# Optimization experiments

Measured on AMD Instinct MI355X. Metric: run time of the kernel, lower is better.

## Reference

```python
import jax, jax.numpy as jnp
import numpy as np

B, Hs, Ws, ENC = 128, 14, 14, 2048
ATT, EMB, DEC, V, L = 512, 512, 512, 30000, 22


def setup_inputs() -> dict:
    key = jax.random.key(0)
    ks = jax.random.split(key, 16)
    u = lambda k, shape, a: jax.random.uniform(k, shape, jnp.float32, -a, a)
    cap_len_rest = jax.random.randint(ks[2], (B - 1, 1), 2, L + 1)
    caption_lengths = jnp.concatenate([jnp.array([[L]], dtype=cap_len_rest.dtype), cap_len_rest], axis=0)
    return {
        "encoder_out": jax.random.normal(ks[0], (B, Hs, Ws, ENC), jnp.float32),
        "encoded_captions": jax.random.randint(ks[1], (B, L), 0, V),
        "caption_lengths": caption_lengths,
        # learned parameters
        "emb_table": u(ks[3], (V, EMB), 0.1),
        "We": u(ks[4], (ENC, ATT), 0.02), "be": jnp.zeros((ATT,), jnp.float32),
        "Wd": u(ks[5], (DEC, ATT), 0.02), "bd": jnp.zeros((ATT,), jnp.float32),
        "wf": u(ks[6], (ATT,), 0.02), "bf": jnp.zeros((), jnp.float32),
        "W_ih": u(ks[7], (4 * DEC, EMB + ENC), 0.02), "b_ih": jnp.zeros((4 * DEC,), jnp.float32),
        "W_hh": u(ks[8], (4 * DEC, DEC), 0.02), "b_hh": jnp.zeros((4 * DEC,), jnp.float32),
        "W_fc": u(ks[9], (DEC, V), 0.1), "b_fc": jnp.zeros((V,), jnp.float32),
    }


def reference(encoder_out, encoded_captions, caption_lengths,
              emb_table, We, be, Wd, bd, wf, bf,
              W_ih, b_ih, W_hh, b_hh, W_fc, b_fc):
    Bsz = encoder_out.shape[0]
    enc = encoder_out.reshape(Bsz, -1, encoder_out.shape[-1])  # [B, P, ENC]
    lens = caption_lengths[:, 0]
    sort_ind = jnp.argsort(-lens)  # descending, stable
    lens = lens[sort_ind]
    enc = enc[sort_ind]
    caps = encoded_captions[sort_ind]
    emb = emb_table[caps]  # [B, L, EMB]
    dec_lens = lens - 1
    T = caps.shape[1] - 1  # static max(decode_lengths) (max length present in batch)
    D = W_hh.shape[1]

    attn1 = enc @ We + be  # [B, P, ATT], loop-invariant
    h0 = jnp.zeros((Bsz, D), enc.dtype)
    c0 = jnp.zeros((Bsz, D), enc.dtype)

    def step(carry, xs):
        h, c = carry
        emb_t, active = xs  # [B, EMB], [B] bool
        attn2 = h @ Wd + bd  # [B, ATT]
        e = jnp.einsum('bpa,a->bp', jax.nn.relu(attn1 + attn2[:, None, :]), wf) + bf
        alpha = jax.nn.softmax(e, axis=1)  # [B, P]
        ctx = jnp.einsum('bp,bpe->be', alpha, enc)  # [B, ENC]
        x = jnp.concatenate([emb_t, ctx], axis=1)
        gates = x @ W_ih.T + b_ih + h @ W_hh.T + b_hh
        i, f, g, o = jnp.split(gates, 4, axis=1)  # PyTorch LSTM gate order
        c_new = jax.nn.sigmoid(f) * c + jax.nn.sigmoid(i) * jnp.tanh(g)
        h_new = jax.nn.sigmoid(o) * jnp.tanh(c_new)
        m = active[:, None]
        h = jnp.where(m, h_new, h)
        c = jnp.where(m, c_new, c)
        out_t = jnp.where(m, h_new @ W_fc + b_fc, 0.0)  # [B, V]
        alpha_t = jnp.where(m, alpha, 0.0)
        return (h, c), (out_t, alpha_t)

    ts = jnp.arange(T)
    active = ts[:, None] < dec_lens[None, :]  # [T, B]
    emb_steps = jnp.transpose(emb[:, :T], (1, 0, 2))  # [T, B, EMB]
    (_, _), (outs, alphas) = jax.lax.scan(step, (h0, c0), (emb_steps, active))
    outputs = jnp.transpose(outs, (1, 0, 2))  # [B, T, V]
    alphas = jnp.transpose(alphas, (1, 0, 2))  # [B, T, P]
    return outputs, caps, dec_lens, alphas, sort_ind
```

## Files before the change

kernel.cpp:

```cpp
#include <hip/hip_runtime.h>
#include <cstdint>
#include <cstddef>

#define B_    128
#define P_    196
#define ENC_  2048
#define ATT_  512
#define DEC_  512
#define EMB_  512
#define V_    30000
#define VPAD_ 30080
#define L_    22
#define T_    21
#define KGATE (EMB_ + ENC_ + DEC_)
#define NGATE (4*DEC_)
#define KS    8
#define LDSK  40

typedef unsigned short u16;
typedef unsigned int   u32;
typedef float f32x4 __attribute__((ext_vector_type(4)));
typedef short s16x8 __attribute__((ext_vector_type(8)));

__device__ __forceinline__ u16 f2bf(float f){
  u32 u = __float_as_uint(f);
  u = (u + 0x7fffu + ((u >> 16) & 1u)) >> 16;
  return (u16)u;
}
__device__ __forceinline__ float bf2f(u16 h){
  return __uint_as_float(((u32)h) << 16);
}

__device__ __forceinline__ void gload_lds16(const u16* g, u16* l){
  __builtin_amdgcn_global_load_lds(
      (const __attribute__((address_space(1))) void*)g,
      (__attribute__((address_space(3))) void*)l, 16, 0, 0);
}

template<int MODE>
__global__ __launch_bounds__(256)
void gemm_bt(const u16* __restrict__ A,
             const u16* __restrict__ Bt,
             int N, int K,
             const float* __restrict__ bias,
             u16* __restrict__ outb,
             float* __restrict__ outp,
             const int* __restrict__ declens)
{
  __shared__ __align__(16) char smem[32768];
  u16 (*As)[128*32] = reinterpret_cast<u16(*)[128*32]>(smem);
  u16 (*Bs)[128*32] = reinterpret_cast<u16(*)[128*32]>(smem + 16384);
  float* Cs = reinterpret_cast<float*>(smem);

  const int tid = threadIdx.x;

  const int nwg = gridDim.x * gridDim.y;
  int lin = blockIdx.y * gridDim.x + blockIdx.x;
  {
    int q = nwg >> 3, r = nwg & 7;
    int xcd = lin & 7, idx = lin >> 3;
    lin = (xcd < r ? xcd * (q + 1) : r * (q + 1) + (xcd - r) * q) + idx;
  }
  int bxn, bym;
  if (MODE == 2){ bym = lin % gridDim.x; bxn = lin / gridDim.x; }
  else          { bxn = lin % gridDim.x; bym = lin / gridDim.x; }
  const int nt = bxn * 128;
  const size_t mt = (size_t)bym * 128;

  const int wv = tid >> 6;
  const int ln = tid & 63;
  const int lm = ln & 15;
  const int qd = ln >> 4;
  const int wr = wv >> 1;
  const int wc = wv & 1;

  f32x4 acc[4][4];
  #pragma unroll
  for (int i=0;i<4;i++)
    #pragma unroll
    for (int j=0;j<4;j++) acc[i][j] = f32x4{0.f,0.f,0.f,0.f};

  const int c0 = tid, c1 = 256 + tid;
  const int ar0 = c0 >> 2, ac0 = (((c0 & 3) ^ ((ar0 >> 1) & 3)) * 8);
  const int ar1 = c1 >> 2, ac1 = (((c1 & 3) ^ ((ar1 >> 1) & 3)) * 8);
  const u16* Ab0 = A  + (mt + ar0) * (size_t)K + ac0;
  const u16* Ab1 = A  + (mt + ar1) * (size_t)K + ac1;
  const u16* Bb0 = Bt + ((size_t)nt + ar0) * (size_t)K + ac0;
  const u16* Bb1 = Bt + ((size_t)nt + ar1) * (size_t)K + ac1;
  const int lo0 = c0 * 8, lo1 = c1 * 8;

  int aoff[4], boff[4];
  #pragma unroll
  for (int i=0;i<4;i++){
    int ra = wr*64 + i*16 + lm;
    aoff[i] = ra*32 + ((qd ^ ((ra >> 1) & 3)) * 8);
    int rb = wc*64 + i*16 + lm;
    boff[i] = rb*32 + ((qd ^ ((rb >> 1) & 3)) * 8);
  }

#define STAGE_(buf, kc) do {                       \
    gload_lds16(Ab0 + (kc), &As[buf][lo0]);        \
    gload_lds16(Ab1 + (kc), &As[buf][lo1]);        \
    gload_lds16(Bb0 + (kc), &Bs[buf][lo0]);        \
    gload_lds16(Bb1 + (kc), &Bs[buf][lo1]);        \
  } while(0)

  STAGE_(0, 0);
  __syncthreads();
  int cur = 0;
  for (int kc = 0; kc < K; kc += 32){
    if (kc + 32 < K) STAGE_(cur ^ 1, kc + 32);
    s16x8 af[4], bfr[4];
    #pragma unroll
    for (int i=0;i<4;i++) af[i]  = *reinterpret_cast<const s16x8*>(&As[cur][aoff[i]]);
    #pragma unroll
    for (int i=0;i<4;i++) bfr[i] = *reinterpret_cast<const s16x8*>(&Bs[cur][boff[i]]);
    #pragma unroll
    for (int i=0;i<4;i++)
      #pragma unroll
      for (int j=0;j<4;j++)
        acc[i][j] = __builtin_amdgcn_mfma_f32_16x16x32_bf16(af[i], bfr[j], acc[i][j], 0, 0, 0);
    __syncthreads();
    cur ^= 1;
  }
#undef STAGE_

  #pragma unroll
  for (int mi=0; mi<4; mi++){
    const int lrb = wr*16 + qd*4;
    #pragma unroll
    for (int ni=0; ni<4; ni++)
      #pragma unroll
      for (int rr=0; rr<4; rr++)
        Cs[(lrb+rr)*132 + wc*64 + ni*16 + lm] = acc[mi][ni][rr];
    __syncthreads();
    const int er = tid >> 3;
    const int ec = (tid & 7) * 16;
    const size_t grow = mt + (size_t)(er >> 4)*64 + mi*16 + (er & 15);
    const float* cr = Cs + er*132 + ec;
    if (MODE == 0){
      __align__(16) u16 pk[16];
      #pragma unroll
      for (int j=0;j<16;j++) pk[j] = f2bf(cr[j] + bias[nt + ec + j]);
      uint4* dst = reinterpret_cast<uint4*>(outb + grow*(size_t)N + nt + ec);
      dst[0] = *reinterpret_cast<uint4*>(pk);
      dst[1] = *reinterpret_cast<uint4*>(pk + 8);
    } else {
      const int ti = (int)(grow >> 7);
      const int bb = (int)(grow & 127);
      const bool act = ti < declens[bb];
      float* dst = outp + ((size_t)bb*T_ + ti)*(size_t)V_ + nt + ec;
      if (nt + 128 <= N){
        #pragma unroll
        for (int j=0;j<4;j++){
          float4 v;
          v.x = act ? cr[4*j+0] + bias[nt+ec+4*j+0] : 0.f;
          v.y = act ? cr[4*j+1] + bias[nt+ec+4*j+1] : 0.f;
          v.z = act ? cr[4*j+2] + bias[nt+ec+4*j+2] : 0.f;
          v.w = act ? cr[4*j+3] + bias[nt+ec+4*j+3] : 0.f;
          reinterpret_cast<float4*>(dst)[j] = v;
        }
      } else {
        #pragma unroll
        for (int j=0;j<16;j++){
          int col = nt + ec + j;
          if (col < N) dst[j] = act ? cr[j] + bias[col] : 0.f;
        }
      }
    }
    __syncthreads();
  }
}

template<int MODE>
__global__ __launch_bounds__(256)
void gemm_bf16(const u16* __restrict__ A, int lda,
               const u16* __restrict__ Bm, int N, int K, int M,
               const float* __restrict__ bias,
               u16* __restrict__ outb,
               float* __restrict__ outp,
               const int* __restrict__ declens)
{
  __shared__ __align__(16) u16 As[64*LDSK];
  __shared__ __align__(16) u16 Bs[64*LDSK];
  __shared__ __align__(16) float Cs[64*68];

  const int tid = threadIdx.x;
  const int nt = blockIdx.x * 64;
  const int mt = blockIdx.y * 64;
  int k0 = 0, k1 = K;
  if (MODE == 1){ int kl = K / KS; k0 = blockIdx.z * kl; k1 = k0 + kl; }

  f32x4 acc[4];
  #pragma unroll
  for (int s = 0; s < 4; s++) acc[s] = f32x4{0.f,0.f,0.f,0.f};

  const int am = tid >> 2;
  const int ak = (tid & 3) * 8;
  const int bk = tid >> 3;
  const int bn = (tid & 7) * 8;
  const int wv = tid >> 6;
  const int ln = tid & 63;
  const int qd = ln >> 4;
  const int lm = ln & 15;

  for (int kc = k0; kc < k1; kc += 32){
    uint4 av = *reinterpret_cast<const uint4*>(A + (size_t)(mt + am) * lda + kc + ak);
    *reinterpret_cast<uint4*>(&As[am * LDSK + ak]) = av;
    u16 bv[8];
    uint4 bq = *reinterpret_cast<const uint4*>(Bm + (size_t)(kc + bk) * N + nt + bn);
    bv[0]=(u16)(bq.x&0xffff); bv[1]=(u16)(bq.x>>16);
    bv[2]=(u16)(bq.y&0xffff); bv[3]=(u16)(bq.y>>16);
    bv[4]=(u16)(bq.z&0xffff); bv[5]=(u16)(bq.z>>16);
    bv[6]=(u16)(bq.w&0xffff); bv[7]=(u16)(bq.w>>16);
    #pragma unroll
    for (int j=0;j<8;j++) Bs[(bn + j) * LDSK + bk] = bv[j];
    __syncthreads();

    s16x8 af = *reinterpret_cast<const s16x8*>(&As[(wv*16 + lm) * LDSK + qd*8]);
    #pragma unroll
    for (int s=0;s<4;s++){
      s16x8 bfr = *reinterpret_cast<const s16x8*>(&Bs[(s*16 + lm) * LDSK + qd*8]);
      acc[s] = __builtin_amdgcn_mfma_f32_16x16x32_bf16(af, bfr, acc[s], 0, 0, 0);
    }
    __syncthreads();
  }

  #pragma unroll
  for (int s=0;s<4;s++)
    #pragma unroll
    for (int r=0;r<4;r++)
      Cs[(wv*16 + qd*4 + r)*68 + s*16 + lm] = acc[s][r];
  __syncthreads();

  const int row = tid >> 2;
  const int cs0 = (tid & 3) * 16;
  if (MODE == 1){
    float* dst = outp + (size_t)blockIdx.z * M * N + (size_t)(mt+row)*N + nt + cs0;
    #pragma unroll
    for (int j=0;j<4;j++){
      float4 v = { Cs[row*68+cs0+4*j], Cs[row*68+cs0+4*j+1],
                   Cs[row*68+cs0+4*j+2], Cs[row*68+cs0+4*j+3] };
      reinterpret_cast<float4*>(dst)[j] = v;
    }
  }
}

__global__ void cvt_bf16(const float* __restrict__ in, u16* __restrict__ out, int n4){
  int i = blockIdx.x * blockDim.x + threadIdx.x;
  int stride = gridDim.x * blockDim.x;
  for (; i < n4; i += stride){
    float4 v = reinterpret_cast<const float4*>(in)[i];
    __align__(8) u16 p[4] = {f2bf(v.x), f2bf(v.y), f2bf(v.z), f2bf(v.w)};
    reinterpret_cast<uint2*>(out)[i] = *reinterpret_cast<uint2*>(p);
  }
}

__global__ void transpose_cvt(const float* __restrict__ in, u16* __restrict__ out,
                              int K, int N)
{
  __shared__ float tile[32][33];
  int n0 = blockIdx.x * 32, k0 = blockIdx.y * 32;
  int tx = threadIdx.x, ty = threadIdx.y;
  #pragma unroll
  for (int j=0;j<4;j++){
    int k = k0 + ty + j*8, n = n0 + tx;
    tile[ty + j*8][tx] = (n < N) ? in[(size_t)k*N + n] : 0.f;
  }
  __syncthreads();
  #pragma unroll
  for (int j=0;j<4;j++){
    int nl = ty + j*8;
    out[(size_t)(n0 + nl)*K + k0 + tx] = f2bf(tile[tx][nl]);
  }
}

__global__ void build_bigb(const float* __restrict__ Wih, const float* __restrict__ Whh,
                           u16* __restrict__ out)
{
  __shared__ float tile[32][33];
  int k0 = blockIdx.x * 32, n0 = blockIdx.y * 32;
  int tx = threadIdx.x, ty = threadIdx.y;
  #pragma unroll
  for (int j=0;j<4;j++){
    int nl = ty + j*8;
    int n = n0 + nl, k = k0 + tx;
    float v = (k0 < 2560) ? Wih[(size_t)n*2560 + k] : Whh[(size_t)n*512 + (k - 2560)];
    tile[nl][tx] = v;
  }
  __syncthreads();
  #pragma unroll
  for (int j=0;j<4;j++){
    int kl = ty + j*8;
    out[(size_t)(k0 + kl)*NGATE + n0 + tx] = f2bf(tile[tx][kl]);
  }
}

__global__ void sort_kernel(const int* __restrict__ cap_len, const int* __restrict__ caps,
                            int* __restrict__ sortind, int* __restrict__ declens,
                            int* __restrict__ caps_s,
                            float* __restrict__ out_caps, float* __restrict__ out_declens,
                            float* __restrict__ out_sortind)
{
  __shared__ int si[B_];
  if (threadIdx.x == 0){
    int cnt = 0;
    for (int v = L_; v >= 0 && cnt < B_; v--)
      for (int b = 0; b < B_; b++)
        if (cap_len[b] == v) si[cnt++] = b;
  }
  __syncthreads();
  for (int i = threadIdx.x; i < B_; i += 256){
    int sb = si[i];
    sortind[i] = sb; out_sortind[i] = (float)sb;
    int dl = cap_len[sb] - 1;
    declens[i] = dl; out_declens[i] = (float)dl;
  }
  for (int i = threadIdx.x; i < B_*L_; i += 256){
    int bb = i / L_;
    int c = caps[si[bb]*L_ + (i % L_)];
    caps_s[i] = c; out_caps[i] = (float)c;
  }
}

__global__ void emb_fill(const float* __restrict__ emb_table, const int* __restrict__ caps_i,
                         u16* __restrict__ xa, int t)
{
  int b = blockIdx.x;
  int cap = caps_i[b*L_ + t];
  for (int k = threadIdx.x; k < EMB_; k += 256)
    xa[(size_t)b*KGATE + k] = f2bf(emb_table[(size_t)cap*EMB_ + k]);
}

__global__ __launch_bounds__(256)
void attn_esm(const u16* __restrict__ attn1, const float* __restrict__ a2dense,
              const float* __restrict__ bd, const float* __restrict__ wf,
              const float* __restrict__ bfp,
              const int* __restrict__ sortind, const int* __restrict__ declens,
              float* __restrict__ alpha_buf, float* __restrict__ out_alphas, int t)
{
  __shared__ float a2[ATT_];
  __shared__ float wfs[ATT_];
  __shared__ float es[P_];
  __shared__ float red[8];
  int b = blockIdx.x, tid = threadIdx.x;
  for (int i = tid; i < ATT_; i += 256){
    a2[i] = bd[i] + a2dense[(size_t)b*ATT_ + i];
    wfs[i] = wf[i];
  }
  __syncthreads();
  int sb = sortind[b];
  const u16* arow = attn1 + (size_t)sb * P_ * ATT_;
  int wv = tid >> 6, ln = tid & 63;
  float bfv = bfp[0];
  for (int i = 0; i < P_/4; i++){
    int p = i*4 + wv;
    uint4 q = *reinterpret_cast<const uint4*>(arow + (size_t)p*ATT_ + ln*8);
    u32 wd_[4] = {q.x, q.y, q.z, q.w};
    float sum = 0.f;
    #pragma unroll
    for (int j=0;j<4;j++){
      int a0 = ln*8 + 2*j;
      float v0 = bf2f((u16)(wd_[j] & 0xffff)) + a2[a0];
      float v1 = bf2f((u16)(wd_[j] >> 16))    + a2[a0+1];
      sum += fmaxf(v0, 0.f) * wfs[a0];
      sum += fmaxf(v1, 0.f) * wfs[a0+1];
    }
    #pragma unroll
    for (int off=32; off; off>>=1) sum += __shfl_xor(sum, off);
    if (ln == 0) es[p] = sum + bfv;
  }
  __syncthreads();
  float m = (tid < P_) ? es[tid] : -1e30f;
  #pragma unroll
  for (int off=32; off; off>>=1) m = fmaxf(m, __shfl_xor(m, off));
  if (ln == 0) red[wv] = m;
  __syncthreads();
  m = fmaxf(fmaxf(red[0],red[1]), fmaxf(red[2],red[3]));
  float ev = (tid < P_) ? expf(es[tid] - m) : 0.f;
  float sm = ev;
  #pragma unroll
  for (int off=32; off; off>>=1) sm += __shfl_xor(sm, off);
  if (ln == 0) red[4+wv] = sm;
  __syncthreads();
  float tot = red[4]+red[5]+red[6]+red[7];
  if (tid < P_){
    float al = ev / tot;
    alpha_buf[b*P_ + tid] = al;
    out_alphas[((size_t)b*T_ + t)*P_ + tid] = (t < declens[b]) ? al : 0.f;
  }
}

__global__ __launch_bounds__(256)
void ctx_kernel(const u16* __restrict__ enc_bf, const float* __restrict__ alpha_buf,
                const int* __restrict__ sortind, u16* __restrict__ xa)
{
  __shared__ float al[P_];
  int b = blockIdx.x, ch = blockIdx.y, tid = threadIdx.x;
  for (int i = tid; i < P_; i += 256) al[i] = alpha_buf[b*P_ + i];
  __syncthreads();
  int sb = sortind[b];
  const u16* eb = enc_bf + (size_t)sb * P_ * ENC_ + ch * 512 + tid * 2;
  float a0=0.f, a1=0.f;
  #pragma unroll 8
  for (int p=0;p<P_;p++){
    u32 q = *reinterpret_cast<const u32*>(eb + (size_t)p * ENC_);
    float w = al[p];
    a0 += w * bf2f((u16)(q & 0xffff));
    a1 += w * bf2f((u16)(q >> 16));
  }
  __align__(4) u16 pk[2] = {f2bf(a0), f2bf(a1)};
  *reinterpret_cast<u32*>(xa + (size_t)b*KGATE + EMB_ + ch*512 + tid*2) =
      *reinterpret_cast<u32*>(pk);
}

__global__ __launch_bounds__(256)
void lstm_kernel(const float* __restrict__ gpart, const float* __restrict__ bih,
                 const float* __restrict__ bhh,
                 float* __restrict__ hf, float* __restrict__ cfb,
                 u16* __restrict__ xa, u16* __restrict__ Hh,
                 const int* __restrict__ declens, const int* __restrict__ caps_i,
                 const float* __restrict__ emb_table,
                 const u16* __restrict__ WdT, float* __restrict__ a2buf, int t)
{
  __shared__ float hs[DEC_];
  int b = blockIdx.x, tid = threadIdx.x;
  bool act = t < declens[b];
  #pragma unroll
  for (int j=0;j<2;j++){
    int n = j*256 + tid;
    float gi = bih[n]      + bhh[n];
    float gf = bih[n+512]  + bhh[n+512];
    float gg = bih[n+1024] + bhh[n+1024];
    float go = bih[n+1536] + bhh[n+1536];
    #pragma unroll
    for (int s=0;s<KS;s++){
      const float* gp = gpart + ((size_t)s*B_ + b)*NGATE;
      gi += gp[n]; gf += gp[n+512]; gg += gp[n+1024]; go += gp[n+1536];
    }
    float co = cfb[b*DEC_ + n];
    float iv = 1.f/(1.f + expf(-gi));
    float fv = 1.f/(1.f + expf(-gf));
    float gv = tanhf(gg);
    float ov = 1.f/(1.f + expf(-go));
    float cn = fv*co + iv*gv;
    float hn = ov * tanhf(cn);
    float ho = act ? hn : hf[b*DEC_ + n];
    float c2 = act ? cn : co;
    hf[b*DEC_ + n] = ho;
    cfb[b*DEC_ + n] = c2;
    u16 hb = f2bf(ho);
    xa[(size_t)b*KGATE + EMB_ + ENC_ + n] = hb;
    Hh[((size_t)t*B_ + b)*DEC_ + n] = hb;
    hs[n] = bf2f(hb);
  }
  if (t + 1 < T_){
    int cap = caps_i[b*L_ + t + 1];
    for (int k = tid; k < EMB_; k += 256)
      xa[(size_t)b*KGATE + k] = f2bf(emb_table[(size_t)cap*EMB_ + k]);
    __syncthreads();
    #pragma unroll
    for (int j=0;j<2;j++){
      int a = j*256 + tid;
      const u16* wr = WdT + (size_t)a * DEC_;
      float s = 0.f;
      for (int k=0;k<DEC_;k+=8){
        uint4 q = *reinterpret_cast<const uint4*>(wr + k);
        u32 ww[4] = {q.x, q.y, q.z, q.w};
        #pragma unroll
        for (int u2=0;u2<4;u2++){
          s += bf2f((u16)(ww[u2] & 0xffff)) * hs[k + 2*u2];
          s += bf2f((u16)(ww[u2] >> 16))    * hs[k + 2*u2 + 1];
        }
      }
      a2buf[(size_t)b*ATT_ + a] = s;
    }
  }
}

extern "C" void kernel_launch(void* const* d_in, const int* in_sizes, int n_in,
                              void* d_out, int out_size, void* d_ws, size_t ws_size,
                              hipStream_t stream)
{
  (void)in_sizes; (void)n_in; (void)out_size; (void)ws_size;
  const float* enc  = (const float*)d_in[0];
  const int*   caps = (const int*)d_in[1];
  const int*   clen = (const int*)d_in[2];
  const float* embt = (const float*)d_in[3];
  const float* We   = (const float*)d_in[4];
  const float* be   = (const float*)d_in[5];
  const float* Wd   = (const float*)d_in[6];
  const float* bd   = (const float*)d_in[7];
  const float* wf   = (const float*)d_in[8];
  const float* bfp  = (const float*)d_in[9];
  const float* Wih  = (const float*)d_in[10];
  const float* bih  = (const float*)d_in[11];
  const float* Whh  = (const float*)d_in[12];
  const float* bhh  = (const float*)d_in[13];
  const float* Wfc  = (const float*)d_in[14];
  const float* bfc  = (const float*)d_in[15];

  float* out = (float*)d_out;
  float* out_outputs = out;
  float* out_caps    = out + (size_t)80640000;
  float* out_declens = out + (size_t)80640000 + 2816;
  float* out_alphas  = out + (size_t)80640000 + 2816 + 128;
  float* out_sortind = out + (size_t)80640000 + 2816 + 128 + 526848;

  char* w = (char*)d_ws;
  size_t off = 0;
  auto alloc = [&](size_t bytes)->char*{
    char* p = w + off; off += (bytes + 255) & ~(size_t)255; return p;
  };
  u16*  enc_bf = (u16*)alloc((size_t)B_*P_*ENC_*2);
  u16*  attn1  = (u16*)alloc((size_t)B_*P_*ATT_*2);
  u16*  WeT    = (u16*)alloc((size_t)ATT_*ENC_*2);
  u16*  WdT    = (u16*)alloc((size_t)ATT_*DEC_*2);
  u16*  BigB   = (u16*)alloc((size_t)KGATE*NGATE*2);
  u16*  WfcT   = (u16*)alloc((size_t)VPAD_*DEC_*2);
  u16*  Hh     = (u16*)alloc((size_t)T_*B_*DEC_*2);
  float* hf    = (float*)alloc((size_t)B_*DEC_*4);
  float* cf    = (float*)alloc((size_t)B_*DEC_*4);
  u16*  xa     = (u16*)alloc((size_t)B_*KGATE*2);
  float* a2buf = (float*)alloc((size_t)B_*ATT_*4);
  float* gp    = (float*)alloc((size_t)KS*B_*NGATE*4);
  float* albuf = (float*)alloc((size_t)B_*P_*4);
  int*  caps_i = (int*)alloc((size_t)B_*L_*4);
  int*  decl_i = (int*)alloc(512);
  int*  sort_i = (int*)alloc(512);

  hipMemsetAsync(hf, 0,
      (size_t)B_*DEC_*4*2 + (size_t)B_*KGATE*2 + (size_t)B_*ATT_*4, stream);

  sort_kernel<<<1, 256, 0, stream>>>(clen, caps, sort_i, decl_i, caps_i,
                                     out_caps, out_declens, out_sortind);
  emb_fill<<<B_, 256, 0, stream>>>(embt, caps_i, xa, 0);

  cvt_bf16<<<4096, 256, 0, stream>>>(enc, enc_bf, (int)((size_t)B_*P_*ENC_/4));
  transpose_cvt<<<dim3(ATT_/32, ENC_/32), dim3(32, 8), 0, stream>>>(We, WeT, ENC_, ATT_);
  transpose_cvt<<<dim3(ATT_/32, DEC_/32), dim3(32, 8), 0, stream>>>(Wd, WdT, DEC_, ATT_);
  transpose_cvt<<<dim3(VPAD_/32, DEC_/32), dim3(32, 8), 0, stream>>>(Wfc, WfcT, DEC_, V_);
  build_bigb<<<dim3(KGATE/32, NGATE/32), dim3(32, 8), 0, stream>>>(Wih, Whh, BigB);

  gemm_bt<0><<<dim3(ATT_/128, (B_*P_)/128), 256, 0, stream>>>(
      enc_bf, WeT, ATT_, ENC_, be, attn1, nullptr, nullptr);

  for (int t = 0; t < T_; t++){
    attn_esm<<<B_, 256, 0, stream>>>(attn1, a2buf, bd, wf, bfp, sort_i, decl_i,
                                     albuf, out_alphas, t);
    ctx_kernel<<<dim3(B_, 4), 256, 0, stream>>>(enc_bf, albuf, sort_i, xa);
    gemm_bf16<1><<<dim3(NGATE/64, B_/64, KS), 256, 0, stream>>>(
        xa, KGATE, BigB, NGATE, KGATE, B_, nullptr, nullptr, gp, nullptr);
    lstm_kernel<<<B_, 256, 0, stream>>>(gp, bih, bhh, hf, cf, xa, Hh,
                                        decl_i, caps_i, embt, WdT, a2buf, t);
  }

  gemm_bt<2><<<dim3((T_*B_)/128, VPAD_/128), 256, 0, stream>>>(
      Hh, WfcT, V_, DEC_, bfc, nullptr, out_outputs, decl_i);
}
```

Baseline: 2.930 ms.

## Fuse per-step decoder kernels into one persistent kernel with grid barriers

Replaces the 84 per-timestep launches (attention, context, gate GEMM, LSTM) with a single persistent 256-block kernel that loops over timesteps and separates phases with atomic-counter grid barriers. The attn2 projection is now computed redundantly by both blocks of each batch row and kept in LDS, which removes the a2buf and alpha buffers. This aims to eliminate launch overhead and inter-kernel gaps on the serial recurrence. The cost is spin-wait barriers that depend on all 256 blocks being co-resident, and the gate GEMM now runs on fewer blocks, each doing two tiles.

```diff
diff --git a/kernel.cpp b/kernel.cpp
--- a/kernel.cpp
+++ b/kernel.cpp
@@ -16,6 +16,7 @@
 #define NGATE (4*DEC_)
 #define KS    8
 #define LDSK  40
+#define NBLK  256
 
 typedef unsigned short u16;
 typedef unsigned int   u32;
@@ -35,6 +36,17 @@
   __builtin_amdgcn_global_load_lds(
       (const __attribute__((address_space(1))) void*)g,
       (__attribute__((address_space(3))) void*)l, 16, 0, 0);
+}
+
+__device__ __forceinline__ void gsync(unsigned* bar, unsigned target){
+  __syncthreads();
+  if (threadIdx.x == 0){
+    __hip_atomic_fetch_add(bar, 1u, __ATOMIC_ACQ_REL, __HIP_MEMORY_SCOPE_AGENT);
+    while (__hip_atomic_load(bar, __ATOMIC_RELAXED, __HIP_MEMORY_SCOPE_AGENT) < target)
+      __builtin_amdgcn_s_sleep(2);
+    __threadfence();
+  }
+  __syncthreads();
 }
 
 template<int MODE>
@@ -172,24 +184,18 @@
   }
 }
 
-template<int MODE>
-__global__ __launch_bounds__(256)
-void gemm_bf16(const u16* __restrict__ A, int lda,
-               const u16* __restrict__ Bm, int N, int K, int M,
-               const float* __restrict__ bias,
-               u16* __restrict__ outb,
-               float* __restrict__ outp,
-               const int* __restrict__ declens)
-{
-  __shared__ __align__(16) u16 As[64*LDSK];
-  __shared__ __align__(16) u16 Bs[64*LDSK];
-  __shared__ __align__(16) float Cs[64*68];
-
-  const int tid = threadIdx.x;
-  const int nt = blockIdx.x * 64;
-  const int mt = blockIdx.y * 64;
-  int k0 = 0, k1 = K;
-  if (MODE == 1){ int kl = K / KS; k0 = blockIdx.z * kl; k1 = k0 + kl; }
+__device__ __forceinline__ void gates_tile(const u16* __restrict__ xa,
+                                           const u16* __restrict__ BigB,
+                                           float* __restrict__ gp,
+                                           int mt, int nt, int z, int tid,
+                                           char* sm)
+{
+  u16* As = reinterpret_cast<u16*>(sm);
+  u16* Bs = reinterpret_cast<u16*>(sm) + 64*LDSK;
+  float* Cs = reinterpret_cast<float*>(sm + 2*64*LDSK*2);
+
+  const int k0 = z * (KGATE/KS);
+  const int k1 = k0 + (KGATE/KS);
 
   f32x4 acc[4];
   #pragma unroll
@@ -205,10 +211,10 @@
   const int lm = ln & 15;
 
   for (int kc = k0; kc < k1; kc += 32){
-    uint4 av = *reinterpret_cast<const uint4*>(A + (size_t)(mt + am) * lda + kc + ak);
+    uint4 av = *reinterpret_cast<const uint4*>(xa + (size_t)(mt + am) * KGATE + kc + ak);
     *reinterpret_cast<uint4*>(&As[am * LDSK + ak]) = av;
     u16 bv[8];
-    uint4 bq = *reinterpret_cast<const uint4*>(Bm + (size_t)(kc + bk) * N + nt + bn);
+    uint4 bq = *reinterpret_cast<const uint4*>(BigB + (size_t)(kc + bk) * NGATE + nt + bn);
     bv[0]=(u16)(bq.x&0xffff); bv[1]=(u16)(bq.x>>16);
     bv[2]=(u16)(bq.y&0xffff); bv[3]=(u16)(bq.y>>16);
     bv[4]=(u16)(bq.z&0xffff); bv[5]=(u16)(bq.z>>16);
@@ -235,229 +241,57 @@
 
   const int row = tid >> 2;
   const int cs0 = (tid & 3) * 16;
-  if (MODE == 1){
-    float* dst = outp + (size_t)blockIdx.z * M * N + (size_t)(mt+row)*N + nt + cs0;
-    #pragma unroll
-    for (int j=0;j<4;j++){
-      float4 v = { Cs[row*68+cs0+4*j], Cs[row*68+cs0+4*j+1],
-                   Cs[row*68+cs0+4*j+2], Cs[row*68+cs0+4*j+3] };
-      reinterpret_cast<float4*>(dst)[j] = v;
-    }
-  }
-}
-
-__global__ void cvt_bf16(const float* __restrict__ in, u16* __restrict__ out, int n4){
-  int i = blockIdx.x * blockDim.x + threadIdx.x;
-  int stride = gridDim.x * blockDim.x;
-  for (; i < n4; i += stride){
-    float4 v = reinterpret_cast<const float4*>(in)[i];
-    __align__(8) u16 p[4] = {f2bf(v.x), f2bf(v.y), f2bf(v.z), f2bf(v.w)};
-    reinterpret_cast<uint2*>(out)[i] = *reinterpret_cast<uint2*>(p);
-  }
-}
-
-__global__ void transpose_cvt(const float* __restrict__ in, u16* __restrict__ out,
-                              int K, int N)
-{
-  __shared__ float tile[32][33];
-  int n0 = blockIdx.x * 32, k0 = blockIdx.y * 32;
-  int tx = threadIdx.x, ty = threadIdx.y;
+  float* dst = gp + ((size_t)z * B_ + (mt + row)) * NGATE + nt + cs0;
   #pragma unroll
   for (int j=0;j<4;j++){
-    int k = k0 + ty + j*8, n = n0 + tx;
-    tile[ty + j*8][tx] = (n < N) ? in[(size_t)k*N + n] : 0.f;
-  }
-  __syncthreads();
-  #pragma unroll
-  for (int j=0;j<4;j++){
-    int nl = ty + j*8;
-    out[(size_t)(n0 + nl)*K + k0 + tx] = f2bf(tile[tx][nl]);
-  }
-}
-
-__global__ void build_bigb(const float* __restrict__ Wih, const float* __restrict__ Whh,
-                           u16* __restrict__ out)
-{
-  __shared__ float tile[32][33];
-  int k0 = blockIdx.x * 32, n0 = blockIdx.y * 32;
-  int tx = threadIdx.x, ty = threadIdx.y;
-  #pragma unroll
-  for (int j=0;j<4;j++){
-    int nl = ty + j*8;
-    int n = n0 + nl, k = k0 + tx;
-    float v = (k0 < 2560) ? Wih[(size_t)n*2560 + k] : Whh[(size_t)n*512 + (k - 2560)];
-    tile[nl][tx] = v;
-  }
-  __syncthreads();
-  #pragma unroll
-  for (int j=0;j<4;j++){
-    int kl = ty + j*8;
-    out[(size_t)(k0 + kl)*NGATE + n0 + tx] = f2bf(tile[tx][kl]);
-  }
-}
-
-__global__ void sort_kernel(const int* __restrict__ cap_len, const int* __restrict__ caps,
-                            int* __restrict__ sortind, int* __restrict__ declens,
-                            int* __restrict__ caps_s,
-                            float* __restrict__ out_caps, float* __restrict__ out_declens,
-                            float* __restrict__ out_sortind)
-{
-  __shared__ int si[B_];
-  if (threadIdx.x == 0){
-    int cnt = 0;
-    for (int v = L_; v >= 0 && cnt < B_; v--)
-      for (int b = 0; b < B_; b++)
-        if (cap_len[b] == v) si[cnt++] = b;
-  }
-  __syncthreads();
-  for (int i = threadIdx.x; i < B_; i += 256){
-    int sb = si[i];
-    sortind[i] = sb; out_sortind[i] = (float)sb;
-    int dl = cap_len[sb] - 1;
-    declens[i] = dl; out_declens[i] = (float)dl;
-  }
-  for (int i = threadIdx.x; i < B_*L_; i += 256){
-    int bb = i / L_;
-    int c = caps[si[bb]*L_ + (i % L_)];
-    caps_s[i] = c; out_caps[i] = (float)c;
-  }
-}
-
-__global__ void emb_fill(const float* __restrict__ emb_table, const int* __restrict__ caps_i,
-                         u16* __restrict__ xa, int t)
-{
-  int b = blockIdx.x;
-  int cap = caps_i[b*L_ + t];
-  for (int k = threadIdx.x; k < EMB_; k += 256)
-    xa[(size_t)b*KGATE + k] = f2bf(emb_table[(size_t)cap*EMB_ + k]);
+    float4 v = { Cs[row*68+cs0+4*j], Cs[row*68+cs0+4*j+1],
+                 Cs[row*68+cs0+4*j+2], Cs[row*68+cs0+4*j+3] };
+    reinterpret_cast<float4*>(dst)[j] = v;
+  }
+  __syncthreads();
 }
 
 __global__ __launch_bounds__(256)
-void attn_esm(const u16* __restrict__ attn1, const float* __restrict__ a2dense,
-              const float* __restrict__ bd, const float* __restrict__ wf,
-              const float* __restrict__ bfp,
-              const int* __restrict__ sortind, const int* __restrict__ declens,
-              float* __restrict__ alpha_buf, float* __restrict__ out_alphas, int t)
-{
-  __shared__ float a2[ATT_];
-  __shared__ float wfs[ATT_];
-  __shared__ float es[P_];
-  __shared__ float red[8];
-  int b = blockIdx.x, tid = threadIdx.x;
-  for (int i = tid; i < ATT_; i += 256){
-    a2[i] = bd[i] + a2dense[(size_t)b*ATT_ + i];
-    wfs[i] = wf[i];
-  }
-  __syncthreads();
-  int sb = sortind[b];
-  const u16* arow = attn1 + (size_t)sb * P_ * ATT_;
-  int wv = tid >> 6, ln = tid & 63;
-  float bfv = bfp[0];
-  for (int i = 0; i < P_/4; i++){
-    int p = i*4 + wv;
-    uint4 q = *reinterpret_cast<const uint4*>(arow + (size_t)p*ATT_ + ln*8);
-    u32 wd_[4] = {q.x, q.y, q.z, q.w};
-    float sum = 0.f;
-    #pragma unroll
-    for (int j=0;j<4;j++){
-      int a0 = ln*8 + 2*j;
-      float v0 = bf2f((u16)(wd_[j] & 0xffff)) + a2[a0];
-      float v1 = bf2f((u16)(wd_[j] >> 16))    + a2[a0+1];
-      sum += fmaxf(v0, 0.f) * wfs[a0];
-      sum += fmaxf(v1, 0.f) * wfs[a0+1];
-    }
-    #pragma unroll
-    for (int off=32; off; off>>=1) sum += __shfl_xor(sum, off);
-    if (ln == 0) es[p] = sum + bfv;
-  }
-  __syncthreads();
-  float m = (tid < P_) ? es[tid] : -1e30f;
-  #pragma unroll
-  for (int off=32; off; off>>=1) m = fmaxf(m, __shfl_xor(m, off));
-  if (ln == 0) red[wv] = m;
-  __syncthreads();
-  m = fmaxf(fmaxf(red[0],red[1]), fmaxf(red[2],red[3]));
-  float ev = (tid < P_) ? expf(es[tid] - m) : 0.f;
-  float sm = ev;
-  #pragma unroll
-  for (int off=32; off; off>>=1) sm += __shfl_xor(sm, off);
-  if (ln == 0) red[4+wv] = sm;
-  __syncthreads();
-  float tot = red[4]+red[5]+red[6]+red[7];
-  if (tid < P_){
-    float al = ev / tot;
-    alpha_buf[b*P_ + tid] = al;
-    out_alphas[((size_t)b*T_ + t)*P_ + tid] = (t < declens[b]) ? al : 0.f;
-  }
-}
-
-__global__ __launch_bounds__(256)
-void ctx_kernel(const u16* __restrict__ enc_bf, const float* __restrict__ alpha_buf,
-                const int* __restrict__ sortind, u16* __restrict__ xa)
-{
-  __shared__ float al[P_];
-  int b = blockIdx.x, ch = blockIdx.y, tid = threadIdx.x;
-  for (int i = tid; i < P_; i += 256) al[i] = alpha_buf[b*P_ + i];
-  __syncthreads();
-  int sb = sortind[b];
-  const u16* eb = enc_bf + (size_t)sb * P_ * ENC_ + ch * 512 + tid * 2;
-  float a0=0.f, a1=0.f;
-  #pragma unroll 8
-  for (int p=0;p<P_;p++){
-    u32 q = *reinterpret_cast<const u32*>(eb + (size_t)p * ENC_);
-    float w = al[p];
-    a0 += w * bf2f((u16)(q & 0xffff));
-    a1 += w * bf2f((u16)(q >> 16));
-  }
-  __align__(4) u16 pk[2] = {f2bf(a0), f2bf(a1)};
-  *reinterpret_cast<u32*>(xa + (size_t)b*KGATE + EMB_ + ch*512 + tid*2) =
-      *reinterpret_cast<u32*>(pk);
-}
-
-__global__ __launch_bounds__(256)
-void lstm_kernel(const float* __restrict__ gpart, const float* __restrict__ bih,
-                 const float* __restrict__ bhh,
-                 float* __restrict__ hf, float* __restrict__ cfb,
-                 u16* __restrict__ xa, u16* __restrict__ Hh,
-                 const int* __restrict__ declens, const int* __restrict__ caps_i,
-                 const float* __restrict__ emb_table,
-                 const u16* __restrict__ WdT, float* __restrict__ a2buf, int t)
-{
-  __shared__ float hs[DEC_];
-  int b = blockIdx.x, tid = threadIdx.x;
-  bool act = t < declens[b];
-  #pragma unroll
-  for (int j=0;j<2;j++){
-    int n = j*256 + tid;
-    float gi = bih[n]      + bhh[n];
-    float gf = bih[n+512]  + bhh[n+512];
-    float gg = bih[n+1024] + bhh[n+1024];
-    float go = bih[n+1536] + bhh[n+1536];
-    #pragma unroll
-    for (int s=0;s<KS;s++){
-      const float* gp = gpart + ((size_t)s*B_ + b)*NGATE;
-      gi += gp[n]; gf += gp[n+512]; gg += gp[n+1024]; go += gp[n+1536];
-    }
-    float co = cfb[b*DEC_ + n];
-    float iv = 1.f/(1.f + expf(-gi));
-    float fv = 1.f/(1.f + expf(-gf));
-    float gv = tanhf(gg);
-    float ov = 1.f/(1.f + expf(-go));
-    float cn = fv*co + iv*gv;
-    float hn = ov * tanhf(cn);
-    float ho = act ? hn : hf[b*DEC_ + n];
-    float c2 = act ? cn : co;
-    hf[b*DEC_ + n] = ho;
-    cfb[b*DEC_ + n] = c2;
-    u16 hb = f2bf(ho);
-    xa[(size_t)b*KGATE + EMB_ + ENC_ + n] = hb;
-    Hh[((size_t)t*B_ + b)*DEC_ + n] = hb;
-    hs[n] = bf2f(hb);
-  }
-  if (t + 1 < T_){
-    int cap = caps_i[b*L_ + t + 1];
-    for (int k = tid; k < EMB_; k += 256)
-      xa[(size_t)b*KGATE + k] = f2bf(emb_table[(size_t)cap*EMB_ + k]);
+void step_loop(const u16* __restrict__ attn1, const u16* __restrict__ enc_bf,
+               const u16* __restrict__ WdT, const u16* __restrict__ BigB,
+               const float* __restrict__ bd, const float* __restrict__ wf,
+               const float* __restrict__ bfp,
+               const float* __restrict__ bih, const float* __restrict__ bhh,
+               const float* __restrict__ embt,
+               const int* __restrict__ caps_i, const int* __restrict__ declens,
+               const int* __restrict__ sortind,
+               float* __restrict__ hf, float* __restrict__ cfb,
+               u16* __restrict__ xa, float* __restrict__ gp,
+               float* __restrict__ out_alphas, u16* __restrict__ Hh,
+               unsigned* __restrict__ bar)
+{
+  __shared__ float al_s[P_];
+  __shared__ __align__(16) char smu[2*64*LDSK*2 + 64*68*4];
+
+  const int tid  = threadIdx.x;
+  const int blk  = blockIdx.x;
+  const int b    = blk >> 1;
+  const int half = blk & 1;
+  const int sb = sortind[b];
+  const int dl = declens[b];
+  const int wv = tid >> 6, ln = tid & 63;
+  const int gnt = (blk >> 3) * 64;
+  const int gz  = blk & 7;
+  unsigned epoch = 0;
+
+  float* hs  = reinterpret_cast<float*>(smu);
+  float* a2  = hs + 512;
+  float* wfs = a2 + 512;
+  float* es  = wfs + 512;
+  float* red = es + 256;
+
+  const float bfv = bfp[0];
+
+  for (int t = 0; t < T_; ++t){
+    hs[tid]        = hf[b*DEC_ + tid];
+    hs[tid + 256]  = hf[b*DEC_ + tid + 256];
+    wfs[tid]       = wf[tid];
+    wfs[tid + 256] = wf[tid + 256];
     __syncthreads();
     #pragma unroll
     for (int j=0;j<2;j++){
@@ -473,9 +307,192 @@
           s += bf2f((u16)(ww[u2] >> 16))    * hs[k + 2*u2 + 1];
         }
       }
-      a2buf[(size_t)b*ATT_ + a] = s;
+      a2[a] = bd[a] + s;
     }
-  }
+    __syncthreads();
+    {
+      const u16* arow = attn1 + (size_t)sb * P_ * ATT_;
+      for (int i = 0; i < P_/4; i++){
+        int p = i*4 + wv;
+        uint4 q = *reinterpret_cast<const uint4*>(arow + (size_t)p*ATT_ + ln*8);
+        u32 wd_[4] = {q.x, q.y, q.z, q.w};
+        float sum = 0.f;
+        #pragma unroll
+        for (int j=0;j<4;j++){
+          int a0 = ln*8 + 2*j;
+          float v0 = bf2f((u16)(wd_[j] & 0xffff)) + a2[a0];
+          float v1 = bf2f((u16)(wd_[j] >> 16))    + a2[a0+1];
+          sum += fmaxf(v0, 0.f) * wfs[a0];
+          sum += fmaxf(v1, 0.f) * wfs[a0+1];
+        }
+        #pragma unroll
+        for (int off=32; off; off>>=1) sum += __shfl_xor(sum, off);
+        if (ln == 0) es[p] = sum + bfv;
+      }
+      __syncthreads();
+      float m = (tid < P_) ? es[tid] : -1e30f;
+      #pragma unroll
+      for (int off=32; off; off>>=1) m = fmaxf(m, __shfl_xor(m, off));
+      if (ln == 0) red[wv] = m;
+      __syncthreads();
+      m = fmaxf(fmaxf(red[0],red[1]), fmaxf(red[2],red[3]));
+      float ev = (tid < P_) ? expf(es[tid] - m) : 0.f;
+      float sm = ev;
+      #pragma unroll
+      for (int off=32; off; off>>=1) sm += __shfl_xor(sm, off);
+      if (ln == 0) red[4+wv] = sm;
+      __syncthreads();
+      float tot = red[4]+red[5]+red[6]+red[7];
+      if (tid < P_){
+        float al = ev / tot;
+        al_s[tid] = al;
+        if (tid >= half*98 && tid < half*98 + 98)
+          out_alphas[((size_t)b*T_ + t)*P_ + tid] = (t < dl) ? al : 0.f;
+      }
+      __syncthreads();
+    }
+    {
+      const u16* eb = enc_bf + (size_t)sb * P_ * ENC_ + half*1024 + tid*4;
+      float c0=0.f, c1=0.f, c2=0.f, c3=0.f;
+      #pragma unroll 4
+      for (int p=0;p<P_;p++){
+        uint2 q = *reinterpret_cast<const uint2*>(eb + (size_t)p * ENC_);
+        float w = al_s[p];
+        c0 += w * bf2f((u16)(q.x & 0xffff));
+        c1 += w * bf2f((u16)(q.x >> 16));
+        c2 += w * bf2f((u16)(q.y & 0xffff));
+        c3 += w * bf2f((u16)(q.y >> 16));
+      }
+      __align__(8) u16 pk[4] = {f2bf(c0), f2bf(c1), f2bf(c2), f2bf(c3)};
+      *reinterpret_cast<uint2*>(xa + (size_t)b*KGATE + EMB_ + half*1024 + tid*4) =
+          *reinterpret_cast<uint2*>(pk);
+    }
+    ++epoch; gsync(bar, epoch * (unsigned)NBLK);
+
+    gates_tile(xa, BigB, gp, 0,  gnt, gz, tid, smu);
+    gates_tile(xa, BigB, gp, 64, gnt, gz, tid, smu);
+    ++epoch; gsync(bar, epoch * (unsigned)NBLK);
+
+    {
+      int n = half*256 + tid;
+      bool act = t < dl;
+      float gi = bih[n]      + bhh[n];
+      float gf = bih[n+512]  + bhh[n+512];
+      float gg = bih[n+1024] + bhh[n+1024];
+      float go = bih[n+1536] + bhh[n+1536];
+      #pragma unroll
+      for (int s=0;s<KS;s++){
+        const float* gpp = gp + ((size_t)s*B_ + b)*NGATE;
+        gi += gpp[n]; gf += gpp[n+512]; gg += gpp[n+1024]; go += gpp[n+1536];
+      }
+      float co = cfb[b*DEC_ + n];
+      float iv = 1.f/(1.f + expf(-gi));
+      float fv = 1.f/(1.f + expf(-gf));
+      float gv = tanhf(gg);
+      float ov = 1.f/(1.f + expf(-go));
+      float cn = fv*co + iv*gv;
+      float hn = ov * tanhf(cn);
+      float ho = act ? hn : hf[b*DEC_ + n];
+      float c2v = act ? cn : co;
+      hf[b*DEC_ + n] = ho;
+      cfb[b*DEC_ + n] = c2v;
+      u16 hb = f2bf(ho);
+      xa[(size_t)b*KGATE + EMB_ + ENC_ + n] = hb;
+      Hh[((size_t)t*B_ + b)*DEC_ + n] = hb;
+      if (t + 1 < T_){
+        int cap = caps_i[b*L_ + t + 1];
+        int k = half*256 + tid;
+        xa[(size_t)b*KGATE + k] = f2bf(embt[(size_t)cap*EMB_ + k]);
+      }
+    }
+    ++epoch; gsync(bar, epoch * (unsigned)NBLK);
+  }
+}
+
+__global__ void cvt_bf16(const float* __restrict__ in, u16* __restrict__ out, int n4){
+  int i = blockIdx.x * blockDim.x + threadIdx.x;
+  int stride = gridDim.x * blockDim.x;
+  for (; i < n4; i += stride){
+    float4 v = reinterpret_cast<const float4*>(in)[i];
+    __align__(8) u16 p[4] = {f2bf(v.x), f2bf(v.y), f2bf(v.z), f2bf(v.w)};
+    reinterpret_cast<uint2*>(out)[i] = *reinterpret_cast<uint2*>(p);
+  }
+}
+
+__global__ void transpose_cvt(const float* __restrict__ in, u16* __restrict__ out,
+                              int K, int N)
+{
+  __shared__ float tile[32][33];
+  int n0 = blockIdx.x * 32, k0 = blockIdx.y * 32;
+  int tx = threadIdx.x, ty = threadIdx.y;
+  #pragma unroll
+  for (int j=0;j<4;j++){
+    int k = k0 + ty + j*8, n = n0 + tx;
+    tile[ty + j*8][tx] = (n < N) ? in[(size_t)k*N + n] : 0.f;
+  }
+  __syncthreads();
+  #pragma unroll
+  for (int j=0;j<4;j++){
+    int nl = ty + j*8;
+    out[(size_t)(n0 + nl)*K + k0 + tx] = f2bf(tile[tx][nl]);
+  }
+}
+
+__global__ void build_bigb(const float* __restrict__ Wih, const float* __restrict__ Whh,
+                           u16* __restrict__ out)
+{
+  __shared__ float tile[32][33];
+  int k0 = blockIdx.x * 32, n0 = blockIdx.y * 32;
+  int tx = threadIdx.x, ty = threadIdx.y;
+  #pragma unroll
+  for (int j=0;j<4;j++){
+    int nl = ty + j*8;
+    int n = n0 + nl, k = k0 + tx;
+    float v = (k0 < 2560) ? Wih[(size_t)n*2560 + k] : Whh[(size_t)n*512 + (k - 2560)];
+    tile[nl][tx] = v;
+  }
+  __syncthreads();
+  #pragma unroll
+  for (int j=0;j<4;j++){
+    int kl = ty + j*8;
+    out[(size_t)(k0 + kl)*NGATE + n0 + tx] = f2bf(tile[tx][kl]);
+  }
+}
+
+__global__ void sort_kernel(const int* __restrict__ cap_len, const int* __restrict__ caps,
+                            int* __restrict__ sortind, int* __restrict__ declens,
+                            int* __restrict__ caps_s,
+                            float* __restrict__ out_caps, float* __restrict__ out_declens,
+                            float* __restrict__ out_sortind)
+{
+  __shared__ int si[B_];
+  if (threadIdx.x == 0){
+    int cnt = 0;
+    for (int v = L_; v >= 0 && cnt < B_; v--)
+      for (int b = 0; b < B_; b++)
+        if (cap_len[b] == v) si[cnt++] = b;
+  }
+  __syncthreads();
+  for (int i = threadIdx.x; i < B_; i += 256){
+    int sb = si[i];
+    sortind[i] = sb; out_sortind[i] = (float)sb;
+    int dl = cap_len[sb] - 1;
+    declens[i] = dl; out_declens[i] = (float)dl;
+  }
+  for (int i = threadIdx.x; i < B_*L_; i += 256){
+    int bb = i / L_;
+    int c = caps[si[bb]*L_ + (i % L_)];
+    caps_s[i] = c; out_caps[i] = (float)c;
+  }
+}
+
+__global__ void emb_fill(const float* __restrict__ emb_table, const int* __restrict__ caps_i,
+                         u16* __restrict__ xa, int t)
+{
+  int b = blockIdx.x;
+  int cap = caps_i[b*L_ + t];
+  for (int k = threadIdx.x; k < EMB_; k += 256)
+    xa[(size_t)b*KGATE + k] = f2bf(emb_table[(size_t)cap*EMB_ + k]);
 }
 
 extern "C" void kernel_launch(void* const* d_in, const int* in_sizes, int n_in,
@@ -522,15 +539,14 @@
   float* hf    = (float*)alloc((size_t)B_*DEC_*4);
   float* cf    = (float*)alloc((size_t)B_*DEC_*4);
   u16*  xa     = (u16*)alloc((size_t)B_*KGATE*2);
-  float* a2buf = (float*)alloc((size_t)B_*ATT_*4);
+  unsigned* bar= (unsigned*)alloc(256);
   float* gp    = (float*)alloc((size_t)KS*B_*NGATE*4);
-  float* albuf = (float*)alloc((size_t)B_*P_*4);
   int*  caps_i = (int*)alloc((size_t)B_*L_*4);
   int*  decl_i = (int*)alloc(512);
   int*  sort_i = (int*)alloc(512);
 
   hipMemsetAsync(hf, 0,
-      (size_t)B_*DEC_*4*2 + (size_t)B_*KGATE*2 + (size_t)B_*ATT_*4, stream);
+      (size_t)B_*DEC_*4*2 + (size_t)B_*KGATE*2 + 256, stream);
 
   sort_kernel<<<1, 256, 0, stream>>>(clen, caps, sort_i, decl_i, caps_i,
                                      out_caps, out_declens, out_sortind);
@@ -545,15 +561,9 @@
   gemm_bt<0><<<dim3(ATT_/128, (B_*P_)/128), 256, 0, stream>>>(
       enc_bf, WeT, ATT_, ENC_, be, attn1, nullptr, nullptr);
 
-  for (int t = 0; t < T_; t++){
-    attn_esm<<<B_, 256, 0, stream>>>(attn1, a2buf, bd, wf, bfp, sort_i, decl_i,
-                                     albuf, out_alphas, t);
-    ctx_kernel<<<dim3(B_, 4), 256, 0, stream>>>(enc_bf, albuf, sort_i, xa);
-    gemm_bf16<1><<<dim3(NGATE/64, B_/64, KS), 256, 0, stream>>>(
-        xa, KGATE, BigB, NGATE, KGATE, B_, nullptr, nullptr, gp, nullptr);
-    lstm_kernel<<<B_, 256, 0, stream>>>(gp, bih, bhh, hf, cf, xa, Hh,
-                                        decl_i, caps_i, embt, WdT, a2buf, t);
-  }
+  step_loop<<<NBLK, 256, 0, stream>>>(
+      attn1, enc_bf, WdT, BigB, bd, wf, bfp, bih, bhh, embt,
+      caps_i, decl_i, sort_i, hf, cf, xa, gp, out_alphas, Hh, bar);
 
   gemm_bt<2><<<dim3((T_*B_)/128, VPAD_/128), 256, 0, stream>>>(
       Hh, WfcT, V_, DEC_, bfc, nullptr, out_outputs, decl_i);
```

New measurement: 4.007 ms. 1.37x slower.
